# Kernel optimization log

Hardware: AMD Instinct MI355X
Metric: run time of the kernel (lower is better)

Reference implementation:

```python
import jax, jax.numpy as jnp
import numpy as np

B, S, E = 8, 2048, 768
N, H = 12, 64
INIT = 0.02
IGNORE = -100000.0


def setup_inputs() -> dict:
    key = jax.random.key(0)
    ks = jax.random.split(key, 5)
    return {
        "normalized_resid_pre": jax.random.normal(ks[0], (B, S, E), jnp.float32),
        "W_Q": jax.random.normal(ks[1], (N, E, H), jnp.float32) * INIT,
        "W_K": jax.random.normal(ks[2], (N, E, H), jnp.float32) * INIT,
        "W_V": jax.random.normal(ks[3], (N, E, H), jnp.float32) * INIT,
        "W_O": jax.random.normal(ks[4], (N, H, E), jnp.float32) * INIT,
        "b_Q": jnp.zeros((N, H), jnp.float32),
        "b_K": jnp.zeros((N, H), jnp.float32),
        "b_V": jnp.zeros((N, H), jnp.float32),
        "b_O": jnp.zeros((E,), jnp.float32),
    }


def reference(normalized_resid_pre, W_Q, W_K, W_V, W_O, b_Q, b_K, b_V, b_O):
    x = normalized_resid_pre
    b, s, e = x.shape
    d_head = W_Q.shape[-1]
    q = jnp.einsum('bse,neh->bsnh', x, W_Q) + b_Q  # [b, sq, n, h]
    k = jnp.einsum('bse,neh->bsnh', x, W_K) + b_K
    v = jnp.einsum('bse,neh->bsnh', x, W_V) + b_V
    scores = jnp.einsum('bqnh,bknh->bnqk', q, k) / jnp.sqrt(jnp.float32(d_head))
    mask = jnp.tril(jnp.ones((s, s), jnp.float32))  # [sq, sk]
    masked = mask * scores + (1.0 - mask) * IGNORE
    probs = jax.nn.softmax(masked, axis=-1)
    z = jnp.einsum('bnqk,bknh->bqnh', probs, v)
    # sum over heads of per-head output projection + bias
    out = jnp.einsum('bqnh,nhe->bqe', z, W_O) + b_O
    return out
```

## Files before the change

kernel.cpp:

```cpp
#include <hip/hip_runtime.h>
#include <hip/hip_bf16.h>
#include <stdint.h>


#define B_ 8
#define S_ 2048
#define E_ 768
#define NHEADS 12
#define HD 64
#define BS (B_*S_)
#define NHD (NHEADS*HD)

typedef short bf16x8 __attribute__((ext_vector_type(8)));
typedef short bf16x4 __attribute__((ext_vector_type(4)));
typedef float f32x4  __attribute__((ext_vector_type(4)));
typedef __hip_bfloat16 bf16;

typedef const __attribute__((address_space(1))) char* as1_t;
typedef __attribute__((address_space(3))) char* as3_t;

__device__ __forceinline__ f32x4 mfma16(bf16x8 a, bf16x8 b, f32x4 c) {
    return __builtin_amdgcn_mfma_f32_16x16x32_bf16(a, b, c, 0, 0, 0);
}
__device__ __forceinline__ bf16x8 ld8(const bf16* p) {
    return *reinterpret_cast<const bf16x8*>(p);
}
__device__ __forceinline__ void gload16(const bf16* g, bf16* l) {
    __builtin_amdgcn_global_load_lds((as1_t)g, (as3_t)l, 16, 0, 0);
}
__device__ __forceinline__ bf16x8 pack8(f32x4 a, f32x4 b) {
    union { bf16x8 v; __hip_bfloat162 h[4]; } u;
    u.h[0] = __float22bfloat162_rn(make_float2(a[0], a[1]));
    u.h[1] = __float22bfloat162_rn(make_float2(a[2], a[3]));
    u.h[2] = __float22bfloat162_rn(make_float2(b[0], b[1]));
    u.h[3] = __float22bfloat162_rn(make_float2(b[2], b[3]));
    return u.v;
}

__global__ __launch_bounds__(256) void prep_kernel(
    const float* __restrict__ x,  const float* __restrict__ Wq,
    const float* __restrict__ Wk, const float* __restrict__ Wv,
    const float* __restrict__ Wo,
    bf16* __restrict__ xb,  bf16* __restrict__ WqT, bf16* __restrict__ WkT,
    bf16* __restrict__ WvT, bf16* __restrict__ WoT)
{
    const int tid = blockIdx.x * 256 + threadIdx.x;
    const int nth = gridDim.x * 256;
    for (int i = tid; i < BS*E_; i += nth)
        xb[i] = __float2bfloat16(x[i]);
    for (int i = tid; i < NHD*E_; i += nth) {
        const int c = i / E_;
        const int e = i - c*E_;
        const int n = c >> 6, h = c & 63;
        const int src = (n*E_ + e)*HD + h;
        WqT[i] = __float2bfloat16(Wq[src]);
        WkT[i] = __float2bfloat16(Wk[src]);
        WvT[i] = __float2bfloat16(Wv[src]);
        WoT[e*NHD + c] = __float2bfloat16(Wo[i]);
    }
}


#define FENCE() asm volatile("" ::: "memory")
#define VMCNT4() asm volatile("s_waitcnt vmcnt(4)" ::: "memory")

#define STG(dst, gbase, kt, rh) do {                                              \
    const bf16* _s = (gbase) + (size_t)((rh)*128 + w*16 + l16)*768 + (kt)*64 + kc8;\
    gload16(_s,      &(dst)[((rh)*2 + 0)*4096 + w*512]);                          \
    gload16(_s + 32, &(dst)[((rh)*2 + 1)*4096 + w*512]);                          \
} while (0)

#define PHASE(bufA, bufB, q, LOADB, STAGE, WAIT) do {                             \
    if (LOADB) {                                                                  \
        _Pragma("unroll") for (int n = 0; n < 4; ++n)                             \
        _Pragma("unroll") for (int ks = 0; ks < 2; ++ks)                          \
            bfr[n][ks] = ld8(&(bufB)[((wn>>1)*2 + ks)*4096 +                      \
                                     ((wn&1)*4 + n)*512 + lane*8]);               \
    }                                                                             \
    bf16x8 afr[2][2];                                                             \
    _Pragma("unroll") for (int m = 0; m < 2; ++m)                                 \
    _Pragma("unroll") for (int ks = 0; ks < 2; ++ks)                              \
        afr[m][ks] = ld8(&(bufA)[(wm*2 + ks)*4096 + ((q)*2 + m)*512 + lane*8]);   \
    STAGE;                                                                        \
    FENCE(); __builtin_amdgcn_s_barrier(); FENCE();                               \
    asm volatile("s_waitcnt lgkmcnt(0)" ::: "memory");                            \
    __builtin_amdgcn_s_setprio(1);                                                \
    _Pragma("unroll") for (int m = 0; m < 2; ++m)                                 \
    _Pragma("unroll") for (int n = 0; n < 4; ++n)                                 \
    _Pragma("unroll") for (int ks = 0; ks < 2; ++ks)                              \
        acc[(q)*2 + m][n] = mfma16(afr[m][ks], bfr[n][ks], acc[(q)*2 + m][n]);    \
    __builtin_amdgcn_s_setprio(0);                                                \
    WAIT;                                                                         \
    FENCE(); __builtin_amdgcn_s_barrier(); FENCE();                               \
} while (0)

#define GEMM256_BODY(Ab, Bb)                                                      \
    f32x4 acc[8][4];                                                              \
    _Pragma("unroll") for (int mf = 0; mf < 8; ++mf)                              \
    _Pragma("unroll") for (int nf = 0; nf < 4; ++nf)                              \
        acc[mf][nf] = (f32x4){0.f, 0.f, 0.f, 0.f};                                \
    bf16x8 bfr[4][2];                                                             \
    STG(sA[0], Ab, 0, 0); STG(sA[0], Ab, 0, 1);                                   \
    STG(sB[0], Bb, 0, 0); STG(sB[0], Bb, 0, 1);                                   \
    STG(sB[1], Bb, 1, 0); STG(sB[1], Bb, 1, 1);                                   \
    VMCNT4();                                                                     \
    FENCE(); __builtin_amdgcn_s_barrier(); FENCE();                               \
    _Pragma("unroll 1")                                                           \
    for (int i = 0; i < 6; ++i) {                                                 \
        const int kA  = 2*i + 1;                                                  \
        const int kN  = (2*i + 2 < 12) ? 2*i + 2 : 11;                            \
        const int kN3 = (2*i + 3 < 12) ? 2*i + 3 : 11;                            \
        PHASE(sA[0], sB[0], 0, 1, STG(sA[1], Ab, kA,  0), (void)0);               \
        PHASE(sA[0], sB[0], 1, 0, STG(sA[1], Ab, kA,  1), (void)0);               \
        PHASE(sA[0], sB[0], 2, 0, STG(sB[0], Bb, kN,  0), (void)0);               \
        PHASE(sA[0], sB[0], 3, 0, STG(sB[0], Bb, kN,  1), VMCNT4());              \
        PHASE(sA[1], sB[1], 0, 1, STG(sA[0], Ab, kN,  0), (void)0);               \
        PHASE(sA[1], sB[1], 1, 0, STG(sA[0], Ab, kN,  1), (void)0);               \
        PHASE(sA[1], sB[1], 2, 0, STG(sB[1], Bb, kN3, 0), (void)0);               \
        PHASE(sA[1], sB[1], 3, 0, STG(sB[1], Bb, kN3, 1), VMCNT4());              \
    }

__global__ __launch_bounds__(512, 2) void qkv_gemm256(
    const bf16* __restrict__ xb, const bf16* __restrict__ WT,
    const float* __restrict__ bq, const float* __restrict__ bk, const float* __restrict__ bv,
    bf16* __restrict__ Qb, bf16* __restrict__ Kb, bf16* __restrict__ VTb)
{
    __shared__ __align__(16) bf16 sA[2][16384];
    __shared__ __align__(16) bf16 sB[2][16384];

    const int tm = blockIdx.x, tn = blockIdx.y;
    const int lane = threadIdx.x & 63;
    const int w    = threadIdx.x >> 6;
    const int wm = w >> 2, wn = w & 3;
    const int l16 = lane & 15, quad = lane >> 4;
    const int kc8 = quad * 8;
    const bf16* Ab = xb + (size_t)tm*256*E_;
    const bf16* Bb = WT + (size_t)tn*256*E_;

    GEMM256_BODY(Ab, Bb);

    const int mat = tn / 3;
    const int cloc0 = (tn - mat*3)*256 + wn*64;
    const float* bias = (mat==0) ? bq : (mat==1) ? bk : bv;
    const float scale = (mat==0) ? 0.125f * 1.44269504088896340736f : 1.0f;
    bf16* dstQK = (mat==0) ? Qb : Kb;
    #pragma unroll
    for (int nf = 0; nf < 4; ++nf) {
        const int col = cloc0 + nf*16 + l16;
        const int hn = col >> 6, h = col & 63;
        const float bb = bias[col];
        #pragma unroll
        for (int mf = 0; mf < 8; ++mf) {
            const int row = tm*256 + wm*128 + mf*16 + quad*4;
            const int bi = row >> 11;
            const int s  = row & (S_-1);
            if (mat < 2) {
                bf16* d = dstQK + ((size_t)(bi*NHEADS + hn)*S_ + s)*HD + h;
                #pragma unroll
                for (int r = 0; r < 4; ++r)
                    d[(size_t)r*HD] = __float2bfloat16((acc[mf][nf][r] + bb)*scale);
            } else {
                bf16* d = VTb + ((size_t)(bi*NHEADS + hn)*HD + h)*S_ + s;
                union { bf16x4 v; bf16 e[4]; } u;
                #pragma unroll
                for (int r = 0; r < 4; ++r) u.e[r] = __float2bfloat16(acc[mf][nf][r] + bb);
                *reinterpret_cast<bf16x4*>(d) = u.v;
            }
        }
    }
}

__global__ __launch_bounds__(512, 2) void out_gemm256(
    const bf16* __restrict__ Z, const bf16* __restrict__ WoT,
    const float* __restrict__ bo, float* __restrict__ out)
{
    __shared__ __align__(16) bf16 sA[2][16384];
    __shared__ __align__(16) bf16 sB[2][16384];

    const int tm = blockIdx.x, tn = blockIdx.y;
    const int lane = threadIdx.x & 63;
    const int w    = threadIdx.x >> 6;
    const int wm = w >> 2, wn = w & 3;
    const int l16 = lane & 15, quad = lane >> 4;
    const int kc8 = quad * 8;
    const bf16* Ab = Z   + (size_t)tm*256*NHD;
    const bf16* Bb = WoT + (size_t)tn*256*NHD;

    GEMM256_BODY(Ab, Bb);

    #pragma unroll
    for (int nf = 0; nf < 4; ++nf) {
        const int col = tn*256 + wn*64 + nf*16 + l16;
        const float bb = bo[col];
        #pragma unroll
        for (int mf = 0; mf < 8; ++mf) {
            const int row = tm*256 + wm*128 + mf*16 + quad*4;
            float* d = out + (size_t)row*E_ + col;
            #pragma unroll
            for (int r = 0; r < 4; ++r)
                d[(size_t)r*E_] = acc[mf][nf][r] + bb;
        }
    }
}

__global__ __launch_bounds__(256, 3) void attn_kernel(
    const bf16* __restrict__ Qb, const bf16* __restrict__ Kb,
    const bf16* __restrict__ VTb, bf16* __restrict__ Z)
{
    __shared__ __align__(16) bf16 sK[2][64*64];
    __shared__ __align__(16) bf16 sV[2][64*64];

    const int id = blockIdx.x;
    const int bx = id / 96;
    const int g  = id - bx*96;
    const int hn = g % NHEADS, b = g / NHEADS;
    const int tid  = threadIdx.x;
    const int w    = tid >> 6;
    const int lane = tid & 63;
    const int l16 = lane & 15, quad = lane >> 4;
    const size_t bn = (size_t)b*NHEADS + hn;

    const bf16* Qbase = Qb  + bn*S_*HD;
    const bf16* Kbase = Kb  + bn*S_*HD;
    const bf16* Vbase = VTb + bn*HD*S_;

    const int mA = tid, mB = tid + 256;
    const int rA = mA >> 3, cgA = mA & 7;
    const int rB = mB >> 3, cgB = mB & 7;
    const int slA = (rA*8 + ((cgA + rA + (rA>>3)) & 7)) * 8;
    const int slB = (rB*8 + ((cgB + rB + (rB>>3)) & 7)) * 8;
    const size_t vofA = (size_t)rA*S_ + cgA*8;
    const size_t vofB = (size_t)rB*S_ + cgB*8;

    const int kperm = (l16 >> 2)*8 + (l16 & 3);
    int kidx[2][2][2];
    #pragma unroll
    for (int c=0;c<2;c++)
        #pragma unroll
        for (int bg=0;bg<2;bg++)
            #pragma unroll
            for (int hf=0;hf<2;hf++) {
                const int r = 32*c + 4*bg + kperm;
                const int q = hf*4 + quad;
                kidx[c][bg][hf] = (r*8 + ((q + r + (r>>3)) & 7)) * 8;
            }
    int vidx[4][2];
    #pragma unroll
    for (int ht=0;ht<4;ht++)
        #pragma unroll
        for (int c=0;c<2;c++) {
            const int rho = ht*16 + l16;
            const int q = c*4 + quad;
            vidx[ht][c] = (rho*8 + ((q + rho + (rho>>3)) & 7)) * 8;
        }

    #pragma unroll
    for (int half = 0; half < 2; ++half) {
        const int qblk = half ? (S_/128 - 1 - bx) : bx;
        const int ktb  = 2*qblk + 1;
        const int ktw  = 2*qblk + (w >> 1);
        const int qbase = qblk*128 + w*32;

        bf16x8 bqf[2][2];
        #pragma unroll
        for (int qi=0;qi<2;qi++)
            #pragma unroll
            for (int hf=0;hf<2;hf++)
                bqf[qi][hf] = ld8(Qbase + (size_t)(qbase + qi*16 + l16)*HD + hf*32 + quad*8);

        f32x4 acc[2][4];
        #pragma unroll
        for (int qi=0;qi<2;qi++)
            #pragma unroll
            for (int ht=0;ht<4;ht++) acc[qi][ht] = (f32x4){0.f,0.f,0.f,0.f};
        float lsum[2] = {0.f, 0.f};

        bf16x8 k0 = ld8(Kbase + (size_t)mA*8);
        bf16x8 k1 = ld8(Kbase + (size_t)mB*8);
        bf16x8 v0 = ld8(Vbase + vofA);
        bf16x8 v1 = ld8(Vbase + vofB);
        *reinterpret_cast<bf16x8*>(&sK[0][slA]) = k0;
        *reinterpret_cast<bf16x8*>(&sK[0][slB]) = k1;
        *reinterpret_cast<bf16x8*>(&sV[0][slA]) = v0;
        *reinterpret_cast<bf16x8*>(&sV[0][slB]) = v1;
        __syncthreads();

        for (int kt = 0; kt <= ktb; ++kt) {
            if (kt < ktb) {
                const size_t kt1 = (size_t)(kt+1)*64;
                k0 = ld8(Kbase + kt1*HD + (size_t)mA*8);
                k1 = ld8(Kbase + kt1*HD + (size_t)mB*8);
                v0 = ld8(Vbase + vofA + kt1);
                v1 = ld8(Vbase + vofB + kt1);
            }
            if (kt <= ktw) {
                const bf16* kb = sK[kt & 1];
                const bf16* vb = sV[kt & 1];
                #pragma unroll
                for (int c=0;c<2;c++) {
                    const bf16x8 akA0 = ld8(kb + kidx[c][0][0]);
                    const bf16x8 akA1 = ld8(kb + kidx[c][0][1]);
                    const bf16x8 akB0 = ld8(kb + kidx[c][1][0]);
                    const bf16x8 akB1 = ld8(kb + kidx[c][1][1]);
                    bf16x8 av[4];
                    #pragma unroll
                    for (int ht=0;ht<4;ht++) av[ht] = ld8(vb + vidx[ht][c]);

                    #pragma unroll
                    for (int qi=0;qi<2;qi++) {
                        f32x4 s0 = (f32x4){0.f,0.f,0.f,0.f};
                        s0 = mfma16(akA0, bqf[qi][0], s0);
                        s0 = mfma16(akA1, bqf[qi][1], s0);
                        f32x4 s1 = (f32x4){0.f,0.f,0.f,0.f};
                        s1 = mfma16(akB0, bqf[qi][0], s1);
                        s1 = mfma16(akB1, bqf[qi][1], s1);
                        if (kt == ktw) {
                            const int q  = qbase + qi*16 + l16;
                            const int kb0 = kt*64 + c*32 + quad*8;
                            #pragma unroll
                            for (int r=0;r<4;r++) {
                                s0[r] = (kb0 + r     > q) ? -1e30f : s0[r];
                                s1[r] = (kb0 + 4 + r > q) ? -1e30f : s1[r];
                            }
                        }
                        float ls = 0.f;
                        #pragma unroll
                        for (int r=0;r<4;r++) {
                            s0[r] = __builtin_amdgcn_exp2f(s0[r]);
                            s1[r] = __builtin_amdgcn_exp2f(s1[r]);
                            ls += s0[r] + s1[r];
                        }
                        lsum[qi] += ls;
                        const bf16x8 pf = pack8(s0, s1);
                        #pragma unroll
                        for (int ht=0;ht<4;ht++)
                            acc[qi][ht] = mfma16(av[ht], pf, acc[qi][ht]);
                    }
                }
            }
            if (kt < ktb) {
                const int nb = (kt+1) & 1;
                *reinterpret_cast<bf16x8*>(&sK[nb][slA]) = k0;
                *reinterpret_cast<bf16x8*>(&sK[nb][slB]) = k1;
                *reinterpret_cast<bf16x8*>(&sV[nb][slA]) = v0;
                *reinterpret_cast<bf16x8*>(&sV[nb][slB]) = v1;
            }
            __syncthreads();
        }

        #pragma unroll
        for (int qi=0;qi<2;qi++) {
            float rs = lsum[qi];
            rs += __shfl_xor(rs, 16, 64);
            rs += __shfl_xor(rs, 32, 64);
            const float inv_l = 1.0f / rs;
            const int q = qbase + qi*16 + l16;
            bf16* zp = Z + ((size_t)b*S_ + q)*NHD + (size_t)hn*HD + quad*4;
            #pragma unroll
            for (int ht=0;ht<4;ht++) {
                union { bf16x4 v; bf16 e[4]; } u;
                #pragma unroll
                for (int r=0;r<4;r++) u.e[r] = __float2bfloat16(acc[qi][ht][r] * inv_l);
                *reinterpret_cast<bf16x4*>(zp + ht*16) = u.v;
            }
        }
    }
}

extern "C" void kernel_launch(void* const* d_in, const int* in_sizes, int n_in,
                              void* d_out, int out_size, void* d_ws, size_t ws_size,
                              hipStream_t stream)
{
    const float* x  = (const float*)d_in[0];
    const float* Wq = (const float*)d_in[1];
    const float* Wk = (const float*)d_in[2];
    const float* Wv = (const float*)d_in[3];
    const float* Wo = (const float*)d_in[4];
    const float* bq = (const float*)d_in[5];
    const float* bk = (const float*)d_in[6];
    const float* bv = (const float*)d_in[7];
    const float* bo = (const float*)d_in[8];
    float* out = (float*)d_out;

    char* ws = (char*)d_ws;
    size_t off = 0;
    auto alloc = [&](size_t bytes){ char* p = ws + off; off += (bytes + 255) & ~(size_t)255; return p; };
    bf16* xb  = (bf16*)alloc((size_t)BS*E_*2);
    bf16* WT  = (bf16*)alloc((size_t)3*NHD*E_*2);
    bf16* WoT = (bf16*)alloc((size_t)E_*NHD*2);
    bf16* Qb  = (bf16*)alloc((size_t)BS*NHD*2);
    bf16* Kb  = (bf16*)alloc((size_t)BS*NHD*2);
    bf16* VTb = (bf16*)alloc((size_t)BS*NHD*2);
    bf16* Zb  = (bf16*)alloc((size_t)BS*NHD*2);

    bf16* WqT = WT;
    bf16* WkT = WT + (size_t)NHD*E_;
    bf16* WvT = WT + (size_t)2*NHD*E_;

    prep_kernel<<<4096, 256, 0, stream>>>(x, Wq, Wk, Wv, Wo, xb, WqT, WkT, WvT, WoT);
    qkv_gemm256<<<dim3(BS/256, 9), 512, 0, stream>>>(xb, WT, bq, bk, bv, Qb, Kb, VTb);
    attn_kernel<<<768, 256, 0, stream>>>(Qb, Kb, VTb, Zb);
    out_gemm256<<<dim3(BS/256, E_/256), 512, 0, stream>>>(Zb, WoT, bo, out);
}
```

Measured before the change: 249.2 us.

## Shrink GEMM N-tile from 256 to 192 to improve CU wave quantization

Changes the QKV and output-projection GEMMs from 256x256 to 256x192 tiles. The staging layout is restructured to three B loads per thread, and the vmcnt waits and shared buffers are adjusted to match. The aim is to fill the 256 CUs more evenly: 256 blocks for the out GEMM and 768 for QKV, instead of 192 and 576 with partial waves. In exchange, each tile does less work per byte of data loaded, so arithmetic intensity is lower.

```diff
diff --git a/kernel.cpp b/kernel.cpp
--- a/kernel.cpp
+++ b/kernel.cpp
@@ -62,31 +62,42 @@
 
 
 #define FENCE() asm volatile("" ::: "memory")
-#define VMCNT4() asm volatile("s_waitcnt vmcnt(4)" ::: "memory")
-
-#define STG(dst, gbase, kt, rh) do {                                              \
-    const bf16* _s = (gbase) + (size_t)((rh)*128 + w*16 + l16)*768 + (kt)*64 + kc8;\
-    gload16(_s,      &(dst)[((rh)*2 + 0)*4096 + w*512]);                          \
-    gload16(_s + 32, &(dst)[((rh)*2 + 1)*4096 + w*512]);                          \
+#define VMCNT3() asm volatile("s_waitcnt vmcnt(3)" ::: "memory")
+
+#define A_ELEM(kh, rg) (((kh)*16 + (rg))*512)
+#define B_ELEM(kh, rg) (((kh)*12 + (rg))*512)
+
+#define STG_A(dst, gbase, kt, kh) do {                                            \
+    const bf16* _s = (gbase) + (size_t)(l16)*768 + (kt)*64 + (kh)*32 + quad*8;    \
+    gload16(_s + (size_t)(w*16)*768,     &(dst)[A_ELEM(kh, w)]);                  \
+    gload16(_s + (size_t)((w+8)*16)*768, &(dst)[A_ELEM(kh, w+8)]);                \
+} while (0)
+
+#define STG_B(dst, gbase, kt) do {                                                \
+    const bf16* _s = (gbase) + (size_t)(l16)*768 + (kt)*64 + quad*8;              \
+    const int _k1 = (w < 4) ? 0 : 1;                                              \
+    const int _r1 = (w < 4) ? (w + 8) : (w - 4);                                  \
+    gload16(_s + (size_t)(w*16)*768,        &(dst)[B_ELEM(0, w)]);                \
+    gload16(_s + (size_t)(_r1*16)*768 + _k1*32, &(dst)[B_ELEM(_k1, _r1)]);        \
+    gload16(_s + (size_t)((w+4)*16)*768 + 32,   &(dst)[B_ELEM(1, w+4)]);          \
 } while (0)
 
 #define PHASE(bufA, bufB, q, LOADB, STAGE, WAIT) do {                             \
     if (LOADB) {                                                                  \
-        _Pragma("unroll") for (int n = 0; n < 4; ++n)                             \
+        _Pragma("unroll") for (int n = 0; n < 3; ++n)                             \
         _Pragma("unroll") for (int ks = 0; ks < 2; ++ks)                          \
-            bfr[n][ks] = ld8(&(bufB)[((wn>>1)*2 + ks)*4096 +                      \
-                                     ((wn&1)*4 + n)*512 + lane*8]);               \
+            bfr[n][ks] = ld8(&(bufB)[((ks)*12 + wn*3 + n)*512 + lane*8]);         \
     }                                                                             \
     bf16x8 afr[2][2];                                                             \
     _Pragma("unroll") for (int m = 0; m < 2; ++m)                                 \
     _Pragma("unroll") for (int ks = 0; ks < 2; ++ks)                              \
-        afr[m][ks] = ld8(&(bufA)[(wm*2 + ks)*4096 + ((q)*2 + m)*512 + lane*8]);   \
+        afr[m][ks] = ld8(&(bufA)[((ks)*16 + wm*8 + (q)*2 + m)*512 + lane*8]);     \
     STAGE;                                                                        \
     FENCE(); __builtin_amdgcn_s_barrier(); FENCE();                               \
     asm volatile("s_waitcnt lgkmcnt(0)" ::: "memory");                            \
     __builtin_amdgcn_s_setprio(1);                                                \
     _Pragma("unroll") for (int m = 0; m < 2; ++m)                                 \
-    _Pragma("unroll") for (int n = 0; n < 4; ++n)                                 \
+    _Pragma("unroll") for (int n = 0; n < 3; ++n)                                 \
     _Pragma("unroll") for (int ks = 0; ks < 2; ++ks)                              \
         acc[(q)*2 + m][n] = mfma16(afr[m][ks], bfr[n][ks], acc[(q)*2 + m][n]);    \
     __builtin_amdgcn_s_setprio(0);                                                \
@@ -94,58 +105,60 @@
     FENCE(); __builtin_amdgcn_s_barrier(); FENCE();                               \
 } while (0)
 
-#define GEMM256_BODY(Ab, Bb)                                                      \
-    f32x4 acc[8][4];                                                              \
+#define GEMM192_BODY(Ab, Bb)                                                      \
+    f32x4 acc[8][3];                                                              \
     _Pragma("unroll") for (int mf = 0; mf < 8; ++mf)                              \
-    _Pragma("unroll") for (int nf = 0; nf < 4; ++nf)                              \
+    _Pragma("unroll") for (int nf = 0; nf < 3; ++nf)                              \
         acc[mf][nf] = (f32x4){0.f, 0.f, 0.f, 0.f};                                \
-    bf16x8 bfr[4][2];                                                             \
-    STG(sA[0], Ab, 0, 0); STG(sA[0], Ab, 0, 1);                                   \
-    STG(sB[0], Bb, 0, 0); STG(sB[0], Bb, 0, 1);                                   \
-    STG(sB[1], Bb, 1, 0); STG(sB[1], Bb, 1, 1);                                   \
-    VMCNT4();                                                                     \
+    bf16x8 bfr[3][2];                                                             \
+    STG_A(sA0, Ab, 0, 0); STG_A(sA0, Ab, 0, 1);                                   \
+    STG_B(sB0, Bb, 0);                                                            \
+    STG_B(sB1, Bb, 1);                                                            \
+    VMCNT3();                                                                     \
     FENCE(); __builtin_amdgcn_s_barrier(); FENCE();                               \
     _Pragma("unroll 1")                                                           \
     for (int i = 0; i < 6; ++i) {                                                 \
         const int kA  = 2*i + 1;                                                  \
         const int kN  = (2*i + 2 < 12) ? 2*i + 2 : 11;                            \
         const int kN3 = (2*i + 3 < 12) ? 2*i + 3 : 11;                            \
-        PHASE(sA[0], sB[0], 0, 1, STG(sA[1], Ab, kA,  0), (void)0);               \
-        PHASE(sA[0], sB[0], 1, 0, STG(sA[1], Ab, kA,  1), (void)0);               \
-        PHASE(sA[0], sB[0], 2, 0, STG(sB[0], Bb, kN,  0), (void)0);               \
-        PHASE(sA[0], sB[0], 3, 0, STG(sB[0], Bb, kN,  1), VMCNT4());              \
-        PHASE(sA[1], sB[1], 0, 1, STG(sA[0], Ab, kN,  0), (void)0);               \
-        PHASE(sA[1], sB[1], 1, 0, STG(sA[0], Ab, kN,  1), (void)0);               \
-        PHASE(sA[1], sB[1], 2, 0, STG(sB[1], Bb, kN3, 0), (void)0);               \
-        PHASE(sA[1], sB[1], 3, 0, STG(sB[1], Bb, kN3, 1), VMCNT4());              \
-    }
+        PHASE(sA0, sB0, 0, 1, STG_A(sA1, Ab, kA, 0), (void)0);                    \
+        PHASE(sA0, sB0, 1, 0, STG_A(sA1, Ab, kA, 1), (void)0);                    \
+        PHASE(sA0, sB0, 2, 0, STG_B(sB0, Bb, kN),    (void)0);                    \
+        PHASE(sA0, sB0, 3, 0, (void)0,               VMCNT3());                   \
+        PHASE(sA1, sB1, 0, 1, STG_A(sA0, Ab, kN, 0), (void)0);                    \
+        PHASE(sA1, sB1, 1, 0, STG_A(sA0, Ab, kN, 1), (void)0);                    \
+        PHASE(sA1, sB1, 2, 0, STG_B(sB1, Bb, kN3),   (void)0);                    \
+        PHASE(sA1, sB1, 3, 0, (void)0,               VMCNT3());                   \
+    }                                                                             \
+    asm volatile("s_waitcnt vmcnt(0)" ::: "memory");
 
 __global__ __launch_bounds__(512, 2) void qkv_gemm256(
     const bf16* __restrict__ xb, const bf16* __restrict__ WT,
     const float* __restrict__ bq, const float* __restrict__ bk, const float* __restrict__ bv,
     bf16* __restrict__ Qb, bf16* __restrict__ Kb, bf16* __restrict__ VTb)
 {
-    __shared__ __align__(16) bf16 sA[2][16384];
-    __shared__ __align__(16) bf16 sB[2][16384];
+    __shared__ __align__(16) bf16 sA0[16384];
+    __shared__ __align__(16) bf16 sA1[16384];
+    __shared__ __align__(16) bf16 sB0[12288];
+    __shared__ __align__(16) bf16 sB1[12288];
 
     const int tm = blockIdx.x, tn = blockIdx.y;
     const int lane = threadIdx.x & 63;
     const int w    = threadIdx.x >> 6;
     const int wm = w >> 2, wn = w & 3;
     const int l16 = lane & 15, quad = lane >> 4;
-    const int kc8 = quad * 8;
     const bf16* Ab = xb + (size_t)tm*256*E_;
-    const bf16* Bb = WT + (size_t)tn*256*E_;
-
-    GEMM256_BODY(Ab, Bb);
-
-    const int mat = tn / 3;
-    const int cloc0 = (tn - mat*3)*256 + wn*64;
+    const bf16* Bb = WT + (size_t)tn*192*E_;
+
+    GEMM192_BODY(Ab, Bb);
+
+    const int mat = tn >> 2;
+    const int cloc0 = (tn & 3)*192 + wn*48;
     const float* bias = (mat==0) ? bq : (mat==1) ? bk : bv;
     const float scale = (mat==0) ? 0.125f * 1.44269504088896340736f : 1.0f;
     bf16* dstQK = (mat==0) ? Qb : Kb;
     #pragma unroll
-    for (int nf = 0; nf < 4; ++nf) {
+    for (int nf = 0; nf < 3; ++nf) {
         const int col = cloc0 + nf*16 + l16;
         const int hn = col >> 6, h = col & 63;
         const float bb = bias[col];
@@ -174,23 +187,24 @@
     const bf16* __restrict__ Z, const bf16* __restrict__ WoT,
     const float* __restrict__ bo, float* __restrict__ out)
 {
-    __shared__ __align__(16) bf16 sA[2][16384];
-    __shared__ __align__(16) bf16 sB[2][16384];
+    __shared__ __align__(16) bf16 sA0[16384];
+    __shared__ __align__(16) bf16 sA1[16384];
+    __shared__ __align__(16) bf16 sB0[12288];
+    __shared__ __align__(16) bf16 sB1[12288];
 
     const int tm = blockIdx.x, tn = blockIdx.y;
     const int lane = threadIdx.x & 63;
     const int w    = threadIdx.x >> 6;
     const int wm = w >> 2, wn = w & 3;
     const int l16 = lane & 15, quad = lane >> 4;
-    const int kc8 = quad * 8;
     const bf16* Ab = Z   + (size_t)tm*256*NHD;
-    const bf16* Bb = WoT + (size_t)tn*256*NHD;
-
-    GEMM256_BODY(Ab, Bb);
+    const bf16* Bb = WoT + (size_t)tn*192*NHD;
+
+    GEMM192_BODY(Ab, Bb);
 
     #pragma unroll
-    for (int nf = 0; nf < 4; ++nf) {
-        const int col = tn*256 + wn*64 + nf*16 + l16;
+    for (int nf = 0; nf < 3; ++nf) {
+        const int col = tn*192 + wn*48 + nf*16 + l16;
         const float bb = bo[col];
         #pragma unroll
         for (int mf = 0; mf < 8; ++mf) {
@@ -398,7 +412,7 @@
     bf16* WvT = WT + (size_t)2*NHD*E_;
 
     prep_kernel<<<4096, 256, 0, stream>>>(x, Wq, Wk, Wv, Wo, xb, WqT, WkT, WvT, WoT);
-    qkv_gemm256<<<dim3(BS/256, 9), 512, 0, stream>>>(xb, WT, bq, bk, bv, Qb, Kb, VTb);
+    qkv_gemm256<<<dim3(BS/256, 12), 512, 0, stream>>>(xb, WT, bq, bk, bv, Qb, Kb, VTb);
     attn_kernel<<<768, 256, 0, stream>>>(Qb, Kb, VTb, Zb);
-    out_gemm256<<<dim3(BS/256, E_/256), 512, 0, stream>>>(Zb, WoT, bo, out);
-}
+    out_gemm256<<<dim3(BS/256, E_/192), 512, 0, stream>>>(Zb, WoT, bo, out);
+}
```

New measurement: 238.2 us. 4.4% less time.
